# Performance work log

Hardware: AMD Instinct MI355X
Metric: run time of the kernel (lower is better)

Reference implementation:

```python
import jax, jax.numpy as jnp
import numpy as np

L, B, T, D, V = 2, 16, 20, 768, 30000


def setup_inputs() -> dict:
    key = jax.random.key(0)
    k1, k2, k3, k4 = jax.random.split(key, 4)
    answer_embed = jax.random.normal(k1, (L, B, T, D), dtype=jnp.float32)
    vocab_embed = 0.1 * jax.random.normal(k2, (V, D), dtype=jnp.float32)
    # classifier_transform modeled as Linear(D, D): y = x @ W.T + b
    W = jax.random.normal(k3, (D, D), dtype=jnp.float32) * (1.0 / np.sqrt(D))
    b = jax.random.normal(k4, (D,), dtype=jnp.float32) * 0.01
    return {"answer_embed": answer_embed, "vocab_embed": vocab_embed, "W": W, "b": b}


def reference(answer_embed, vocab_embed, W, b):
    # vocab_classifiers: [V, D] after the linear transform
    vocab_classifiers = vocab_embed @ W.T + b
    # Original: broadcast multiply [L,B,T,D,1]*[1,1,1,D,V] then sum over D.
    # Mathematically identical contraction over D -> [L, B, T, V]
    return jnp.einsum('lbtd,vd->lbtv', answer_embed, vocab_classifiers)
```

## Files before the change

### kernel.cpp

```cpp
#include <hip/hip_runtime.h>

#define KDIM 768
#define MANS 640
#define VV   30000
#define NGRP 235

typedef __attribute__((ext_vector_type(4)))  float  f32x4;
typedef __attribute__((ext_vector_type(16))) float  f32x16;
typedef __attribute__((ext_vector_type(8)))  __bf16 bf16x8;

__device__ __forceinline__ unsigned short f2bf(float f) {
    union { float f; unsigned int u; } v; v.f = f;
    unsigned int r = v.u + 0x7fffu + ((v.u >> 16) & 1u);
    return (unsigned short)(r >> 16);
}

__device__ __forceinline__ void load_lds16(const unsigned short* g, unsigned short* l) {
    __builtin_amdgcn_global_load_lds(
        (__attribute__((address_space(1))) void*)(void*)g,
        (__attribute__((address_space(3))) void*)l,
        16, 0, 0);
}

__global__ __launch_bounds__(256) void prep_small(
    const float* __restrict__ W, const float* __restrict__ A,
    const float* __restrict__ b, unsigned short* __restrict__ Wt_bf,
    float* __restrict__ cvec)
{
    __shared__ float ts[64][65];
    const int blk = blockIdx.x;
    if (blk < 144) {
        int bx = (blk % 12) * 64, by = (blk / 12) * 64;
        int tx = threadIdx.x & 63, tg = threadIdx.x >> 6;
#pragma unroll
        for (int i = 0; i < 16; ++i) {
            int r = tg * 16 + i;
            ts[r][tx] = W[(long)(by + r) * KDIM + bx + tx];
        }
        __syncthreads();
#pragma unroll
        for (int i = 0; i < 16; ++i) {
            int r = tg * 16 + i;
            Wt_bf[(long)(bx + r) * KDIM + by + tx] = f2bf(ts[tx][r]);
        }
    } else {
        int row  = (blk - 144) * 4 + (threadIdx.x >> 6);
        int lane = threadIdx.x & 63;
        const float* ap = A + (long)row * KDIM;
        float s = 0.f;
#pragma unroll
        for (int i = 0; i < KDIM / 64; ++i) s += ap[i * 64 + lane] * b[i * 64 + lane];
#pragma unroll
        for (int off = 32; off; off >>= 1) s += __shfl_down(s, off, 64);
        if (lane == 0) cvec[row] = s;
    }
}

__global__ __launch_bounds__(256) void gemm_a2(
    const float* __restrict__ Af, const unsigned short* __restrict__ Bp,
    unsigned short* __restrict__ outp)
{
    constexpr int TM = 64, TN = 128;
    __shared__ unsigned short sA[TM * 64];
    __shared__ unsigned short sB[TN * 64];

    const int t    = threadIdx.x;
    const int lane = t & 63;
    const int w    = t >> 6;
    const int wm   = w >> 1;
    const int wn   = w & 1;
    const int half = lane >> 5;
    const int col  = lane & 31;
    const long m0  = (long)blockIdx.x * TM;
    const long n0  = (long)blockIdx.y * TN;

    f32x16 acc[1][2];
    acc[0][0] = (f32x16)(0.f);
    acc[0][1] = (f32x16)(0.f);

    for (int k0 = 0; k0 < KDIM; k0 += 64) {
#pragma unroll
        for (int j = 0; j < 2; ++j) {
            int s   = (j * 4 + w) * 64 + lane;
            int row = s >> 3;
            int c   = (s & 7) ^ (row & 7);
            const float* g = Af + (m0 + row) * KDIM + k0 + c * 8;
            f32x4 v0 = ((const f32x4*)g)[0], v1 = ((const f32x4*)g)[1];
            ushort4 o0, o1;
            o0.x = f2bf(v0.x); o0.y = f2bf(v0.y); o0.z = f2bf(v0.z); o0.w = f2bf(v0.w);
            o1.x = f2bf(v1.x); o1.y = f2bf(v1.y); o1.z = f2bf(v1.z); o1.w = f2bf(v1.w);
            unsigned short* d = &sA[s * 8];
            ((ushort4*)d)[0] = o0; ((ushort4*)d)[1] = o1;
        }
#pragma unroll
        for (int j = 0; j < 4; ++j) {
            int s   = (j * 4 + w) * 64 + lane;
            int row = s >> 3;
            int c   = (s & 7) ^ (row & 7);
            load_lds16(Bp + (n0 + row) * KDIM + k0 + c * 8,
                       &sB[(j * 4 + w) * 64 * 8]);
        }
        __syncthreads();

#pragma unroll
        for (int g = 0; g < 4; ++g) {
            const int cg = g * 2 + half;
            int arow = wm * 32 + col;
            bf16x8 af = *(const bf16x8*)&sA[(arow * 8 + (cg ^ (arow & 7))) * 8];
#pragma unroll
            for (int fn = 0; fn < 2; ++fn) {
                int brow = wn * 64 + fn * 32 + col;
                bf16x8 bf = *(const bf16x8*)&sB[(brow * 8 + (cg ^ (brow & 7))) * 8];
                acc[0][fn] = __builtin_amdgcn_mfma_f32_32x32x16_bf16(
                    af, bf, acc[0][fn], 0, 0, 0);
            }
        }
        __syncthreads();
    }

#pragma unroll
    for (int fn = 0; fn < 2; ++fn) {
        long n = n0 + wn * 64 + fn * 32 + col;
#pragma unroll
        for (int rg = 0; rg < 16; ++rg) {
            long m = m0 + wm * 32 + (rg & 3) + 8 * (rg >> 2) + 4 * half;
            outp[m * KDIM + n] = f2bf(acc[0][fn][rg]);
        }
    }
}

__global__ __launch_bounds__(256) void gemm_big(
    const unsigned short* __restrict__ A, const float* __restrict__ Bf,
    const float* __restrict__ cvec, float* __restrict__ outp)
{
    const int id    = blockIdx.x;
    const int x     = id & 7;
    const int q     = id >> 3;
    const int m_idx = q % 5;
    const int n_grp = (q / 5) * 8 + x;
    if (n_grp >= NGRP) return;

    __shared__ unsigned short sA[128 * 64];
    __shared__ unsigned short sB[128 * 64];

    const int t    = threadIdx.x;
    const int lane = t & 63;
    const int w    = t >> 6;
    const int wm   = w >> 1;
    const int wn   = w & 1;
    const int half = lane >> 5;
    const int col  = lane & 31;
    const long m0  = (long)m_idx * 128;
    const long n0  = (long)n_grp * 128;

    f32x16 acc[2][2];
#pragma unroll
    for (int i = 0; i < 2; ++i)
#pragma unroll
        for (int j = 0; j < 2; ++j) acc[i][j] = (f32x16)(0.f);

    const unsigned short* ga[4];
    unsigned short*       la[4];
#pragma unroll
    for (int j = 0; j < 4; ++j) {
        int s  = (j * 4 + w) * 64 + lane;
        int row = s >> 3;
        int c   = (s & 7) ^ (row & 7);
        ga[j] = A + (m0 + row) * KDIM + c * 8;
        la[j] = &sA[(j * 4 + w) * 64 * 8];
    }
    const float* gb[4];
    unsigned short* lb[4];
#pragma unroll
    for (int j = 0; j < 4; ++j) {
        int s   = j * 256 + t;
        int row = s >> 3;
        int c   = (s & 7) ^ (row & 7);
        long grow = n0 + row;
        if (grow > VV - 1) grow = VV - 1;
        gb[j] = Bf + grow * KDIM + c * 8;
        lb[j] = &sB[s * 8];
    }

    for (int k0 = 0; k0 < KDIM; k0 += 64) {
#pragma unroll
        for (int j = 0; j < 4; ++j) load_lds16(ga[j] + k0, la[j]);
#pragma unroll
        for (int j = 0; j < 4; ++j) {
            const float* g = gb[j] + k0;
            f32x4 v0 = ((const f32x4*)g)[0], v1 = ((const f32x4*)g)[1];
            ushort4 o0, o1;
            o0.x = f2bf(v0.x); o0.y = f2bf(v0.y); o0.z = f2bf(v0.z); o0.w = f2bf(v0.w);
            o1.x = f2bf(v1.x); o1.y = f2bf(v1.y); o1.z = f2bf(v1.z); o1.w = f2bf(v1.w);
            ((ushort4*)lb[j])[0] = o0; ((ushort4*)lb[j])[1] = o1;
        }
        __syncthreads();

#pragma unroll
        for (int g = 0; g < 4; ++g) {
            const int cg = g * 2 + half;
            bf16x8 af[2], bfr[2];
#pragma unroll
            for (int fm = 0; fm < 2; ++fm) {
                int row = wm * 64 + fm * 32 + col;
                af[fm]  = *(const bf16x8*)&sA[(row * 8 + (cg ^ (row & 7))) * 8];
            }
#pragma unroll
            for (int fn = 0; fn < 2; ++fn) {
                int row = wn * 64 + fn * 32 + col;
                bfr[fn] = *(const bf16x8*)&sB[(row * 8 + (cg ^ (row & 7))) * 8];
            }
#pragma unroll
            for (int fm = 0; fm < 2; ++fm)
#pragma unroll
                for (int fn = 0; fn < 2; ++fn)
                    acc[fm][fn] = __builtin_amdgcn_mfma_f32_32x32x16_bf16(
                        af[fm], bfr[fn], acc[fm][fn], 0, 0, 0);
        }
        __syncthreads();
    }

#pragma unroll
    for (int fm = 0; fm < 2; ++fm)
#pragma unroll
        for (int fn = 0; fn < 2; ++fn) {
            long n = n0 + wn * 64 + fn * 32 + col;
            if (n < VV) {
#pragma unroll
                for (int rg = 0; rg < 16; ++rg) {
                    long m = m0 + wm * 64 + fm * 32
                           + (rg & 3) + 8 * (rg >> 2) + 4 * half;
                    outp[m * (long)VV + n] = acc[fm][fn][rg] + cvec[m];
                }
            }
        }
}

extern "C" void kernel_launch(void* const* d_in, const int* in_sizes, int n_in,
                              void* d_out, int out_size, void* d_ws, size_t ws_size,
                              hipStream_t stream) {
    const float* answer = (const float*)d_in[0];
    const float* vocab  = (const float*)d_in[1];
    const float* W      = (const float*)d_in[2];
    const float* bvec   = (const float*)d_in[3];

    char* ws = (char*)d_ws;
    unsigned short* Wt_bf = (unsigned short*)ws;
    unsigned short* A2_bf = (unsigned short*)(ws + 1179648);
    float*          cptr  = (float*)(ws + 1179648 + 983040);

    prep_small<<<304, 256, 0, stream>>>(W, answer, bvec, Wt_bf, cptr);

    gemm_a2<<<dim3(MANS / 64, KDIM / 128), 256, 0, stream>>>(answer, Wt_bf, A2_bf);

    gemm_big<<<1200, 256, 0, stream>>>(A2_bf, vocab, cptr, (float*)d_out);
}
```

Measured before the change: 230.8 us.

## Double-buffer LDS tiles in both GEMMs to overlap loads with MFMA

Both GEMM kernels now keep two LDS buffers. The next K-tile is fetched (direct-to-LDS loads and fp32 register loads) before the MFMA work on the current tile runs, and the bf16 conversion is stored after it. This removes one barrier per iteration and hides global load latency behind compute. In exchange LDS use doubles, to 64KB per block in gemm_big, and register pressure rises from the prefetched fp32 values, which could lower occupancy.

```diff
diff --git a/kernel.cpp b/kernel.cpp
--- a/kernel.cpp
+++ b/kernel.cpp
@@ -4,15 +4,24 @@
 #define MANS 640
 #define VV   30000
 #define NGRP 235
+#define NKS  (KDIM / 64)
 
 typedef __attribute__((ext_vector_type(4)))  float  f32x4;
 typedef __attribute__((ext_vector_type(16))) float  f32x16;
 typedef __attribute__((ext_vector_type(8)))  __bf16 bf16x8;
+typedef __attribute__((ext_vector_type(8)))  unsigned short ushort8;
 
 __device__ __forceinline__ unsigned short f2bf(float f) {
     union { float f; unsigned int u; } v; v.f = f;
     unsigned int r = v.u + 0x7fffu + ((v.u >> 16) & 1u);
     return (unsigned short)(r >> 16);
+}
+
+__device__ __forceinline__ ushort8 cvt8(f32x4 a, f32x4 b) {
+    ushort8 o;
+    o[0] = f2bf(a.x); o[1] = f2bf(a.y); o[2] = f2bf(a.z); o[3] = f2bf(a.w);
+    o[4] = f2bf(b.x); o[5] = f2bf(b.y); o[6] = f2bf(b.z); o[7] = f2bf(b.w);
+    return o;
 }
 
 __device__ __forceinline__ void load_lds16(const unsigned short* g, unsigned short* l) {
@@ -61,8 +70,8 @@
     unsigned short* __restrict__ outp)
 {
     constexpr int TM = 64, TN = 128;
-    __shared__ unsigned short sA[TM * 64];
-    __shared__ unsigned short sB[TN * 64];
+    __shared__ unsigned short sA[2][TM * 64];
+    __shared__ unsigned short sB[2][TN * 64];
 
     const int t    = threadIdx.x;
     const int lane = t & 63;
@@ -74,49 +83,83 @@
     const long m0  = (long)blockIdx.x * TM;
     const long n0  = (long)blockIdx.y * TN;
 
-    f32x16 acc[1][2];
-    acc[0][0] = (f32x16)(0.f);
-    acc[0][1] = (f32x16)(0.f);
-
-    for (int k0 = 0; k0 < KDIM; k0 += 64) {
-#pragma unroll
-        for (int j = 0; j < 2; ++j) {
-            int s   = (j * 4 + w) * 64 + lane;
-            int row = s >> 3;
-            int c   = (s & 7) ^ (row & 7);
-            const float* g = Af + (m0 + row) * KDIM + k0 + c * 8;
-            f32x4 v0 = ((const f32x4*)g)[0], v1 = ((const f32x4*)g)[1];
-            ushort4 o0, o1;
-            o0.x = f2bf(v0.x); o0.y = f2bf(v0.y); o0.z = f2bf(v0.z); o0.w = f2bf(v0.w);
-            o1.x = f2bf(v1.x); o1.y = f2bf(v1.y); o1.z = f2bf(v1.z); o1.w = f2bf(v1.w);
-            unsigned short* d = &sA[s * 8];
-            ((ushort4*)d)[0] = o0; ((ushort4*)d)[1] = o1;
-        }
-#pragma unroll
-        for (int j = 0; j < 4; ++j) {
-            int s   = (j * 4 + w) * 64 + lane;
-            int row = s >> 3;
-            int c   = (s & 7) ^ (row & 7);
-            load_lds16(Bp + (n0 + row) * KDIM + k0 + c * 8,
-                       &sB[(j * 4 + w) * 64 * 8]);
-        }
-        __syncthreads();
-
+    f32x16 acc[2];
+    acc[0] = (f32x16)(0.f);
+    acc[1] = (f32x16)(0.f);
+
+    const float* gaf[2]; int laOff[2];
+#pragma unroll
+    for (int j = 0; j < 2; ++j) {
+        int s   = (j * 4 + w) * 64 + lane;
+        int row = s >> 3;
+        int c   = (s & 7) ^ (row & 7);
+        gaf[j]  = Af + (m0 + row) * KDIM + c * 8;
+        laOff[j] = s * 8;
+    }
+    const unsigned short* gb[4]; unsigned short* lbB[4];
+#pragma unroll
+    for (int j = 0; j < 4; ++j) {
+        int s   = (j * 4 + w) * 64 + lane;
+        int row = s >> 3;
+        int c   = (s & 7) ^ (row & 7);
+        gb[j]  = Bp + (n0 + row) * KDIM + c * 8;
+        lbB[j] = &sB[0][(j * 4 + w) * 64 * 8];
+    }
+
+    auto compute = [&](int pp) {
+        const unsigned short* bA = &sA[0][0] + pp * (TM * 64);
+        const unsigned short* bB = &sB[0][0] + pp * (TN * 64);
 #pragma unroll
         for (int g = 0; g < 4; ++g) {
             const int cg = g * 2 + half;
             int arow = wm * 32 + col;
-            bf16x8 af = *(const bf16x8*)&sA[(arow * 8 + (cg ^ (arow & 7))) * 8];
+            bf16x8 af = *(const bf16x8*)&bA[(arow * 8 + (cg ^ (arow & 7))) * 8];
 #pragma unroll
             for (int fn = 0; fn < 2; ++fn) {
                 int brow = wn * 64 + fn * 32 + col;
-                bf16x8 bf = *(const bf16x8*)&sB[(brow * 8 + (cg ^ (brow & 7))) * 8];
-                acc[0][fn] = __builtin_amdgcn_mfma_f32_32x32x16_bf16(
-                    af, bf, acc[0][fn], 0, 0, 0);
+                bf16x8 bfv = *(const bf16x8*)&bB[(brow * 8 + (cg ^ (brow & 7))) * 8];
+                acc[fn] = __builtin_amdgcn_mfma_f32_32x32x16_bf16(
+                    af, bfv, acc[fn], 0, 0, 0);
             }
         }
+    };
+
+#pragma unroll
+    for (int j = 0; j < 4; ++j) load_lds16(gb[j], lbB[j]);
+    {
+        f32x4 ra[4];
+#pragma unroll
+        for (int j = 0; j < 2; ++j) {
+            ra[2 * j]     = ((const f32x4*)gaf[j])[0];
+            ra[2 * j + 1] = ((const f32x4*)gaf[j])[1];
+        }
+#pragma unroll
+        for (int j = 0; j < 2; ++j)
+            *(ushort8*)(&sA[0][0] + laOff[j]) = cvt8(ra[2 * j], ra[2 * j + 1]);
+    }
+    __syncthreads();
+
+    int p = 0;
+    for (int kt = 0; kt < NKS - 1; ++kt) {
+        const int kn = (kt + 1) * 64;
+        const int oB = (p ^ 1) * (TN * 64);
+        const int oA = (p ^ 1) * (TM * 64);
+#pragma unroll
+        for (int j = 0; j < 4; ++j) load_lds16(gb[j] + kn, lbB[j] + oB);
+        f32x4 ra[4];
+#pragma unroll
+        for (int j = 0; j < 2; ++j) {
+            ra[2 * j]     = ((const f32x4*)(gaf[j] + kn))[0];
+            ra[2 * j + 1] = ((const f32x4*)(gaf[j] + kn))[1];
+        }
+        compute(p);
+#pragma unroll
+        for (int j = 0; j < 2; ++j)
+            *(ushort8*)(&sA[0][0] + oA + laOff[j]) = cvt8(ra[2 * j], ra[2 * j + 1]);
         __syncthreads();
-    }
+        p ^= 1;
+    }
+    compute(p);
 
 #pragma unroll
     for (int fn = 0; fn < 2; ++fn) {
@@ -124,7 +167,7 @@
 #pragma unroll
         for (int rg = 0; rg < 16; ++rg) {
             long m = m0 + wm * 32 + (rg & 3) + 8 * (rg >> 2) + 4 * half;
-            outp[m * KDIM + n] = f2bf(acc[0][fn][rg]);
+            outp[m * KDIM + n] = f2bf(acc[fn][rg]);
         }
     }
 }
@@ -140,8 +183,8 @@
     const int n_grp = (q / 5) * 8 + x;
     if (n_grp >= NGRP) return;
 
-    __shared__ unsigned short sA[128 * 64];
-    __shared__ unsigned short sB[128 * 64];
+    __shared__ unsigned short sA[2][128 * 64];
+    __shared__ unsigned short sB[2][128 * 64];
 
     const int t    = threadIdx.x;
     const int lane = t & 63;
@@ -160,17 +203,16 @@
         for (int j = 0; j < 2; ++j) acc[i][j] = (f32x16)(0.f);
 
     const unsigned short* ga[4];
-    unsigned short*       la[4];
+    unsigned short*       laA[4];
 #pragma unroll
     for (int j = 0; j < 4; ++j) {
-        int s  = (j * 4 + w) * 64 + lane;
+        int s   = (j * 4 + w) * 64 + lane;
         int row = s >> 3;
         int c   = (s & 7) ^ (row & 7);
-        ga[j] = A + (m0 + row) * KDIM + c * 8;
-        la[j] = &sA[(j * 4 + w) * 64 * 8];
-    }
-    const float* gb[4];
-    unsigned short* lb[4];
+        ga[j]  = A + (m0 + row) * KDIM + c * 8;
+        laA[j] = &sA[0][(j * 4 + w) * 64 * 8];
+    }
+    const float* gb[4]; int lbOff[4];
 #pragma unroll
     for (int j = 0; j < 4; ++j) {
         int s   = j * 256 + t;
@@ -178,24 +220,13 @@
         int c   = (s & 7) ^ (row & 7);
         long grow = n0 + row;
         if (grow > VV - 1) grow = VV - 1;
-        gb[j] = Bf + grow * KDIM + c * 8;
-        lb[j] = &sB[s * 8];
-    }
-
-    for (int k0 = 0; k0 < KDIM; k0 += 64) {
-#pragma unroll
-        for (int j = 0; j < 4; ++j) load_lds16(ga[j] + k0, la[j]);
-#pragma unroll
-        for (int j = 0; j < 4; ++j) {
-            const float* g = gb[j] + k0;
-            f32x4 v0 = ((const f32x4*)g)[0], v1 = ((const f32x4*)g)[1];
-            ushort4 o0, o1;
-            o0.x = f2bf(v0.x); o0.y = f2bf(v0.y); o0.z = f2bf(v0.z); o0.w = f2bf(v0.w);
-            o1.x = f2bf(v1.x); o1.y = f2bf(v1.y); o1.z = f2bf(v1.z); o1.w = f2bf(v1.w);
-            ((ushort4*)lb[j])[0] = o0; ((ushort4*)lb[j])[1] = o1;
-        }
-        __syncthreads();
-
+        gb[j]   = Bf + grow * KDIM + c * 8;
+        lbOff[j] = s * 8;
+    }
+
+    auto compute = [&](int pp) {
+        const unsigned short* bA = &sA[0][0] + pp * (128 * 64);
+        const unsigned short* bB = &sB[0][0] + pp * (128 * 64);
 #pragma unroll
         for (int g = 0; g < 4; ++g) {
             const int cg = g * 2 + half;
@@ -203,12 +234,12 @@
 #pragma unroll
             for (int fm = 0; fm < 2; ++fm) {
                 int row = wm * 64 + fm * 32 + col;
-                af[fm]  = *(const bf16x8*)&sA[(row * 8 + (cg ^ (row & 7))) * 8];
+                af[fm] = *(const bf16x8*)&bA[(row * 8 + (cg ^ (row & 7))) * 8];
             }
 #pragma unroll
             for (int fn = 0; fn < 2; ++fn) {
                 int row = wn * 64 + fn * 32 + col;
-                bfr[fn] = *(const bf16x8*)&sB[(row * 8 + (cg ^ (row & 7))) * 8];
+                bfr[fn] = *(const bf16x8*)&bB[(row * 8 + (cg ^ (row & 7))) * 8];
             }
 #pragma unroll
             for (int fm = 0; fm < 2; ++fm)
@@ -217,8 +248,43 @@
                     acc[fm][fn] = __builtin_amdgcn_mfma_f32_32x32x16_bf16(
                         af[fm], bfr[fn], acc[fm][fn], 0, 0, 0);
         }
+    };
+
+#pragma unroll
+    for (int j = 0; j < 4; ++j) load_lds16(ga[j], laA[j]);
+    {
+        f32x4 rb[8];
+#pragma unroll
+        for (int j = 0; j < 4; ++j) {
+            rb[2 * j]     = ((const f32x4*)gb[j])[0];
+            rb[2 * j + 1] = ((const f32x4*)gb[j])[1];
+        }
+#pragma unroll
+        for (int j = 0; j < 4; ++j)
+            *(ushort8*)(&sB[0][0] + lbOff[j]) = cvt8(rb[2 * j], rb[2 * j + 1]);
+    }
+    __syncthreads();
+
+    int p = 0;
+    for (int kt = 0; kt < NKS - 1; ++kt) {
+        const int kn = (kt + 1) * 64;
+        const int o1 = (p ^ 1) * (128 * 64);
+#pragma unroll
+        for (int j = 0; j < 4; ++j) load_lds16(ga[j] + kn, laA[j] + o1);
+        f32x4 nb[8];
+#pragma unroll
+        for (int j = 0; j < 4; ++j) {
+            nb[2 * j]     = ((const f32x4*)(gb[j] + kn))[0];
+            nb[2 * j + 1] = ((const f32x4*)(gb[j] + kn))[1];
+        }
+        compute(p);
+#pragma unroll
+        for (int j = 0; j < 4; ++j)
+            *(ushort8*)(&sB[0][0] + o1 + lbOff[j]) = cvt8(nb[2 * j], nb[2 * j + 1]);
         __syncthreads();
-    }
+        p ^= 1;
+    }
+    compute(p);
 
 #pragma unroll
     for (int fm = 0; fm < 2; ++fm)
```

Result: slower. 250.3 us (+8.4%).

## Pre-convert vocab to bf16 in gemm_a2 blocks and load via direct LDS

Applied to the files above, without the earlier changes.

Adds extra blocks to the gemm_a2 launch that convert the whole fp32 vocab matrix to bf16 in workspace once. gemm_big then loads both operands with global_load_lds instead of reading fp32 and converting in registers. Each vocab tile is reused by 5 M-blocks, so this removes repeated conversion work and halves that operand's global read traffic. It also switches f2bf to hardware bf16 conversion with vectorised 8-wide stores. In exchange it adds a separate write and re-read of a ~46MB bf16 copy of the vocab matrix.

```diff
diff --git a/kernel.cpp b/kernel.cpp
--- a/kernel.cpp
+++ b/kernel.cpp
@@ -4,15 +4,28 @@
 #define MANS 640
 #define VV   30000
 #define NGRP 235
+#define VELEM (VV * KDIM)
+#define CVTBLK ((VELEM + 8191) / 8192)
+#define A2BLK  ((MANS / 64) * (KDIM / 128))
 
 typedef __attribute__((ext_vector_type(4)))  float  f32x4;
 typedef __attribute__((ext_vector_type(16))) float  f32x16;
 typedef __attribute__((ext_vector_type(8)))  __bf16 bf16x8;
+typedef __attribute__((ext_vector_type(8)))  unsigned short ushort8;
 
 __device__ __forceinline__ unsigned short f2bf(float f) {
-    union { float f; unsigned int u; } v; v.f = f;
-    unsigned int r = v.u + 0x7fffu + ((v.u >> 16) & 1u);
-    return (unsigned short)(r >> 16);
+    union { __bf16 h; unsigned short u; } t;
+    t.h = (__bf16)f;
+    return t.u;
+}
+
+__device__ __forceinline__ ushort8 cvt8(f32x4 a, f32x4 b) {
+    union { bf16x8 h; ushort8 u; } c;
+    c.h[0] = (__bf16)a.x; c.h[1] = (__bf16)a.y;
+    c.h[2] = (__bf16)a.z; c.h[3] = (__bf16)a.w;
+    c.h[4] = (__bf16)b.x; c.h[5] = (__bf16)b.y;
+    c.h[6] = (__bf16)b.z; c.h[7] = (__bf16)b.w;
+    return c.u;
 }
 
 __device__ __forceinline__ void load_lds16(const unsigned short* g, unsigned short* l) {
@@ -58,8 +71,23 @@
 
 __global__ __launch_bounds__(256) void gemm_a2(
     const float* __restrict__ Af, const unsigned short* __restrict__ Bp,
-    unsigned short* __restrict__ outp)
+    unsigned short* __restrict__ outp,
+    const float* __restrict__ vocab, unsigned short* __restrict__ vocab_bf)
 {
+    if (blockIdx.x >= A2BLK) {
+        const long base = (long)(blockIdx.x - A2BLK) * 8192 + (long)threadIdx.x * 8;
+#pragma unroll
+        for (int p = 0; p < 4; ++p) {
+            long idx = base + p * 2048;
+            if (idx < VELEM) {
+                f32x4 v0 = ((const f32x4*)(vocab + idx))[0];
+                f32x4 v1 = ((const f32x4*)(vocab + idx))[1];
+                *(ushort8*)(vocab_bf + idx) = cvt8(v0, v1);
+            }
+        }
+        return;
+    }
+
     constexpr int TM = 64, TN = 128;
     __shared__ unsigned short sA[TM * 64];
     __shared__ unsigned short sB[TN * 64];
@@ -71,34 +99,40 @@
     const int wn   = w & 1;
     const int half = lane >> 5;
     const int col  = lane & 31;
-    const long m0  = (long)blockIdx.x * TM;
-    const long n0  = (long)blockIdx.y * TN;
-
-    f32x16 acc[1][2];
-    acc[0][0] = (f32x16)(0.f);
-    acc[0][1] = (f32x16)(0.f);
+    const long m0  = (long)(blockIdx.x % (MANS / 64)) * TM;
+    const long n0  = (long)(blockIdx.x / (MANS / 64)) * TN;
+
+    f32x16 acc[2];
+    acc[0] = (f32x16)(0.f);
+    acc[1] = (f32x16)(0.f);
+
+    const float* gaf[2]; int laOff[2];
+#pragma unroll
+    for (int j = 0; j < 2; ++j) {
+        int s   = (j * 4 + w) * 64 + lane;
+        int row = s >> 3;
+        int c   = (s & 7) ^ (row & 7);
+        gaf[j]   = Af + (m0 + row) * KDIM + c * 8;
+        laOff[j] = s * 8;
+    }
+    const unsigned short* gb[4]; unsigned short* lbB[4];
+#pragma unroll
+    for (int j = 0; j < 4; ++j) {
+        int s   = (j * 4 + w) * 64 + lane;
+        int row = s >> 3;
+        int c   = (s & 7) ^ (row & 7);
+        gb[j]  = Bp + (n0 + row) * KDIM + c * 8;
+        lbB[j] = &sB[(j * 4 + w) * 64 * 8];
+    }
 
     for (int k0 = 0; k0 < KDIM; k0 += 64) {
 #pragma unroll
+        for (int j = 0; j < 4; ++j) load_lds16(gb[j] + k0, lbB[j]);
+#pragma unroll
         for (int j = 0; j < 2; ++j) {
-            int s   = (j * 4 + w) * 64 + lane;
-            int row = s >> 3;
-            int c   = (s & 7) ^ (row & 7);
-            const float* g = Af + (m0 + row) * KDIM + k0 + c * 8;
-            f32x4 v0 = ((const f32x4*)g)[0], v1 = ((const f32x4*)g)[1];
-            ushort4 o0, o1;
-            o0.x = f2bf(v0.x); o0.y = f2bf(v0.y); o0.z = f2bf(v0.z); o0.w = f2bf(v0.w);
-            o1.x = f2bf(v1.x); o1.y = f2bf(v1.y); o1.z = f2bf(v1.z); o1.w = f2bf(v1.w);
-            unsigned short* d = &sA[s * 8];
-            ((ushort4*)d)[0] = o0; ((ushort4*)d)[1] = o1;
-        }
-#pragma unroll
-        for (int j = 0; j < 4; ++j) {
-            int s   = (j * 4 + w) * 64 + lane;
-            int row = s >> 3;
-            int c   = (s & 7) ^ (row & 7);
-            load_lds16(Bp + (n0 + row) * KDIM + k0 + c * 8,
-                       &sB[(j * 4 + w) * 64 * 8]);
+            f32x4 v0 = ((const f32x4*)(gaf[j] + k0))[0];
+            f32x4 v1 = ((const f32x4*)(gaf[j] + k0))[1];
+            *(ushort8*)(&sA[0] + laOff[j]) = cvt8(v0, v1);
         }
         __syncthreads();
 
@@ -110,9 +144,9 @@
 #pragma unroll
             for (int fn = 0; fn < 2; ++fn) {
                 int brow = wn * 64 + fn * 32 + col;
-                bf16x8 bf = *(const bf16x8*)&sB[(brow * 8 + (cg ^ (brow & 7))) * 8];
-                acc[0][fn] = __builtin_amdgcn_mfma_f32_32x32x16_bf16(
-                    af, bf, acc[0][fn], 0, 0, 0);
+                bf16x8 bfv = *(const bf16x8*)&sB[(brow * 8 + (cg ^ (brow & 7))) * 8];
+                acc[fn] = __builtin_amdgcn_mfma_f32_32x32x16_bf16(
+                    af, bfv, acc[fn], 0, 0, 0);
             }
         }
         __syncthreads();
@@ -124,13 +158,13 @@
 #pragma unroll
         for (int rg = 0; rg < 16; ++rg) {
             long m = m0 + wm * 32 + (rg & 3) + 8 * (rg >> 2) + 4 * half;
-            outp[m * KDIM + n] = f2bf(acc[0][fn][rg]);
+            outp[m * KDIM + n] = f2bf(acc[fn][rg]);
         }
     }
 }
 
 __global__ __launch_bounds__(256) void gemm_big(
-    const unsigned short* __restrict__ A, const float* __restrict__ Bf,
+    const unsigned short* __restrict__ A, const unsigned short* __restrict__ Bbf,
     const float* __restrict__ cvec, float* __restrict__ outp)
 {
     const int id    = blockIdx.x;
@@ -160,40 +194,33 @@
         for (int j = 0; j < 2; ++j) acc[i][j] = (f32x16)(0.f);
 
     const unsigned short* ga[4];
-    unsigned short*       la[4];
+    unsigned short*       laA[4];
 #pragma unroll
     for (int j = 0; j < 4; ++j) {
-        int s  = (j * 4 + w) * 64 + lane;
-        int row = s >> 3;
-        int c   = (s & 7) ^ (row & 7);
-        ga[j] = A + (m0 + row) * KDIM + c * 8;
-        la[j] = &sA[(j * 4 + w) * 64 * 8];
-    }
-    const float* gb[4];
-    unsigned short* lb[4];
+        int s   = (j * 4 + w) * 64 + lane;
+        int row = s >> 3;
+        int c   = (s & 7) ^ (row & 7);
+        ga[j]  = A + (m0 + row) * KDIM + c * 8;
+        laA[j] = &sA[(j * 4 + w) * 64 * 8];
+    }
+    const unsigned short* gb[4];
+    unsigned short*       laB[4];
 #pragma unroll
     for (int j = 0; j < 4; ++j) {
-        int s   = j * 256 + t;
+        int s   = (j * 4 + w) * 64 + lane;
         int row = s >> 3;
         int c   = (s & 7) ^ (row & 7);
         long grow = n0 + row;
         if (grow > VV - 1) grow = VV - 1;
-        gb[j] = Bf + grow * KDIM + c * 8;
-        lb[j] = &sB[s * 8];
+        gb[j]  = Bbf + grow * KDIM + c * 8;
+        laB[j] = &sB[(j * 4 + w) * 64 * 8];
     }
 
     for (int k0 = 0; k0 < KDIM; k0 += 64) {
 #pragma unroll
-        for (int j = 0; j < 4; ++j) load_lds16(ga[j] + k0, la[j]);
-#pragma unroll
-        for (int j = 0; j < 4; ++j) {
-            const float* g = gb[j] + k0;
-            f32x4 v0 = ((const f32x4*)g)[0], v1 = ((const f32x4*)g)[1];
-            ushort4 o0, o1;
-            o0.x = f2bf(v0.x); o0.y = f2bf(v0.y); o0.z = f2bf(v0.z); o0.w = f2bf(v0.w);
-            o1.x = f2bf(v1.x); o1.y = f2bf(v1.y); o1.z = f2bf(v1.z); o1.w = f2bf(v1.w);
-            ((ushort4*)lb[j])[0] = o0; ((ushort4*)lb[j])[1] = o1;
-        }
+        for (int j = 0; j < 4; ++j) load_lds16(ga[j] + k0, laA[j]);
+#pragma unroll
+        for (int j = 0; j < 4; ++j) load_lds16(gb[j] + k0, laB[j]);
         __syncthreads();
 
 #pragma unroll
@@ -203,7 +230,7 @@
 #pragma unroll
             for (int fm = 0; fm < 2; ++fm) {
                 int row = wm * 64 + fm * 32 + col;
-                af[fm]  = *(const bf16x8*)&sA[(row * 8 + (cg ^ (row & 7))) * 8];
+                af[fm] = *(const bf16x8*)&sA[(row * 8 + (cg ^ (row & 7))) * 8];
             }
 #pragma unroll
             for (int fn = 0; fn < 2; ++fn) {
@@ -245,13 +272,14 @@
     const float* bvec   = (const float*)d_in[3];
 
     char* ws = (char*)d_ws;
-    unsigned short* Wt_bf = (unsigned short*)ws;
-    unsigned short* A2_bf = (unsigned short*)(ws + 1179648);
-    float*          cptr  = (float*)(ws + 1179648 + 983040);
+    unsigned short* Wt_bf   = (unsigned short*)ws;
+    unsigned short* A2_bf   = (unsigned short*)(ws + 1179648);
+    float*          cptr    = (float*)(ws + 1179648 + 983040);
+    unsigned short* vocabbf = (unsigned short*)(ws + 2165248);
 
     prep_small<<<304, 256, 0, stream>>>(W, answer, bvec, Wt_bf, cptr);
 
-    gemm_a2<<<dim3(MANS / 64, KDIM / 128), 256, 0, stream>>>(answer, Wt_bf, A2_bf);
-
-    gemm_big<<<1200, 256, 0, stream>>>(A2_bf, vocab, cptr, (float*)d_out);
-}
+    gemm_a2<<<A2BLK + CVTBLK, 256, 0, stream>>>(answer, Wt_bf, A2_bf, vocab, vocabbf);
+
+    gemm_big<<<1200, 256, 0, stream>>>(A2_bf, vocabbf, cptr, (float*)d_out);
+}
```

Measured after the change: 222.2 us. 1.04x faster.
